# Performance work log

Measured on AMD Instinct MI355X. Metric: run time of the kernel, lower is better.

The kernel has to match this reference:

```python
import jax, jax.numpy as jnp
import numpy as np

ORDER = 2
BN_EPS = 1e-5

def setup_inputs() -> dict:
    key = jax.random.key(0)
    ks = jax.random.split(key, 8)
    B, N, L, H = 32, 512, 12, 64
    S = 2                      # support_len
    OUT = 64                   # out_dim
    M = ORDER * S * H          # einsum middle dim = 256
    x = jax.random.normal(ks[0], (B, N, L, H), dtype=jnp.float32)
    # row-scaled random diffusion matrices to keep multi-hop propagation stable
    support = jax.random.uniform(ks[1], (S, N, N), dtype=jnp.float32) / N
    scale = 1.0 / M
    weight = scale * jax.random.normal(ks[2], (L, M, OUT), dtype=jnp.float32)
    eps = jnp.zeros((1,), dtype=jnp.float32)
    gamma = jnp.ones((OUT,), dtype=jnp.float32)
    beta = jnp.zeros((OUT,), dtype=jnp.float32)
    w2 = jax.random.normal(ks[3], (OUT, OUT), dtype=jnp.float32) / np.sqrt(OUT)
    b2 = jnp.zeros((OUT,), dtype=jnp.float32)
    return {"x": x, "support": support, "weight": weight, "eps": eps,
            "gamma": gamma, "beta": beta, "w2": w2, "b2": b2}

def reference(x, support, weight, eps, gamma, beta, w2, b2):
    B, N, L, H = x.shape
    xv = x.reshape(B, N, L * H)            # [B,N,LH]
    res = []
    for i in range(support.shape[0]):      # small fixed loop over supports
        A = support[i]                     # [N,N]
        out = xv
        for _ in range(ORDER):
            out = (1.0 + eps) * out + jnp.einsum('nm,bmd->bnd', A, out)
            res.append(out)
    out = jnp.stack(res, axis=-1)          # [B,N,LH,K], K = order*support_len
    K = out.shape[-1]
    out = out.reshape(B, N, L, H * K)      # [B,N,L,M]
    out = jnp.einsum('bnlm,lmo->bno', out, weight)   # [B,N,OUT]
    # dropout is identity in eval mode
    C = out.shape[-1]
    flat = out.reshape(B * N, C)
    mean = flat.mean(axis=0)
    var = flat.var(axis=0)                 # biased, matching torch BN training
    normed = (flat - mean) * jax.lax.rsqrt(var + BN_EPS) * gamma + beta
    y = jax.nn.relu(normed.reshape(B, N, C))
    return jnp.einsum('bnc,oc->bno', y, w2) + b2
```

## Files before the change

kernel.cpp:

```cpp
#include <hip/hip_runtime.h>
#include <hip/hip_bf16.h>
#include <cstddef>
#include <cstdint>

#define B_   32
#define N_   512
#define D_   768
#define OUT_ 64
#define R_   (B_ * N_)

typedef unsigned short u16;
typedef __bf16 bf16x8 __attribute__((ext_vector_type(8)));
typedef float  f32x4  __attribute__((ext_vector_type(4)));
typedef unsigned short u16x8 __attribute__((ext_vector_type(8)));

__device__ __forceinline__ u16 f2bf(float f) {
    __hip_bfloat16 h = __float2bfloat16(f);
    return __builtin_bit_cast(u16, h);
}

__device__ __forceinline__ f32x4 mfma16(u16x8 a, u16x8 b, f32x4 c) {
    return __builtin_amdgcn_mfma_f32_16x16x32_bf16(
        __builtin_bit_cast(bf16x8, a), __builtin_bit_cast(bf16x8, b), c, 0, 0, 0);
}

__device__ __forceinline__ void gl2lds16(const void* g, void* l) {
    __builtin_amdgcn_global_load_lds(
        (const __attribute__((address_space(1))) unsigned int*)g,
        (__attribute__((address_space(3))) unsigned int*)l, 16, 0, 0);
}

__global__ __launch_bounds__(256) void prep2(
    const float* __restrict__ support, const float* __restrict__ weight,
    const float* __restrict__ epsp,
    u16* __restrict__ MallC, u16* __restrict__ MT, u16* __restrict__ Wt)
{
    const int blk = blockIdx.x, tid = threadIdx.x;
    __shared__ float t[32][33];
    if (blk < 512) {
        int s = blk >> 8, rem = blk & 255;
        int n0 = (rem >> 4) * 32, m0 = (rem & 15) * 32;
        const float f = 1.0f + epsp[0];
        const float* S = support + (size_t)s * 262144;
#pragma unroll
        for (int p = 0; p < 4; ++p) {
            int nl = p * 8 + (tid >> 5), ml = tid & 31;
            float v = S[(size_t)(n0 + nl) * 512 + m0 + ml];
            if (n0 + nl == m0 + ml) v += f;
            MallC[(size_t)(n0 + nl) * 2048 + s * 1024 + m0 + ml] = f2bf(v);
            t[nl][ml] = v;
        }
        __syncthreads();
#pragma unroll
        for (int p = 0; p < 4; ++p) {
            int ml = p * 8 + (tid >> 5), nl = tid & 31;
            MT[(size_t)s * 262144 + (size_t)(m0 + ml) * 512 + n0 + nl] = f2bf(t[nl][ml]);
        }
    } else {
        int idx = (blk - 512) * 256 + tid;
        int k = idx / 49152, rem = idx % 49152;
        int o = rem / 768, d = rem % 768;
        int l = d >> 6, hh = d & 63;
        Wt[idx] = f2bf(weight[((size_t)l * 256 + hh * 4 + k) * 64 + o]);
    }
}

__global__ __launch_bounds__(256, 4) void zmsq(
    const u16* __restrict__ Wt, const float* __restrict__ x,
    const u16* __restrict__ MallC_in, const u16* __restrict__ MT,
    u16* __restrict__ Z, u16* __restrict__ MallC_out)
{
    __shared__ __align__(16) u16 SM[16384];
    const int tid = threadIdx.x, lane = tid & 63, wid = tid >> 6;
    const int wr = wid >> 1, wc = wid & 1;
    const int lrow = lane & 15, lk8 = (lane >> 4) * 8;
    const int q = lane >> 4;
    const int bid = blockIdx.x;

    f32x4 acc[2][2] = {};

    if (bid < 1024) {
        const int k = (bid >> 3) & 3;
        const int r2 = (bid >> 5) * 8 + (bid & 7);
        const int b = r2 >> 3, m0 = (r2 & 7) * 64;

        const u16* gsrcA[2]; u16* ldstA[2];
#pragma unroll
        for (int t = 0; t < 2; ++t) {
            int idx = wid * 2 + t;
            int p = idx >> 2, sub = idx & 3;
            gsrcA[t] = Wt + (size_t)(k * 64 + sub * 16 + lrow) * 768 + p * 32 + lk8;
            ldstA[t] = SM + p * 2048 + sub * 512;
        }
        const int r = tid >> 2, c4 = tid & 3;
        const float* gx = x + (size_t)(b * 512 + m0 + r) * 768 + c4 * 16;
        u16* bdst = SM + 4096 + (c4 >> 1) * 2048 + (r >> 4) * 512
                  + (c4 & 1) * 256 + (r & 15) * 8;

        {
            f32x4 a0 = *(const f32x4*)(gx);
            f32x4 a1 = *(const f32x4*)(gx + 4);
            f32x4 a2 = *(const f32x4*)(gx + 8);
            f32x4 a3 = *(const f32x4*)(gx + 12);
#pragma unroll
            for (int t = 0; t < 2; ++t) gl2lds16(gsrcA[t], ldstA[t]);
            u16x8 w0, w1;
#pragma unroll
            for (int j = 0; j < 4; ++j) {
                w0[j] = f2bf(a0[j]); w0[4 + j] = f2bf(a1[j]);
                w1[j] = f2bf(a2[j]); w1[4 + j] = f2bf(a3[j]);
            }
            *(u16x8*)(bdst)       = w0;
            *(u16x8*)(bdst + 128) = w1;
        }
        __syncthreads();

#pragma unroll 2
        for (int kk = 0; kk < 12; ++kk) {
            const int cb = (kk & 1) * 8192, nb = cb ^ 8192;
            f32x4 a0, a1, a2, a3;
            if (kk < 11) {
                const float* g = gx + (kk + 1) * 64;
                a0 = *(const f32x4*)(g);
                a1 = *(const f32x4*)(g + 4);
                a2 = *(const f32x4*)(g + 8);
                a3 = *(const f32x4*)(g + 12);
#pragma unroll
                for (int t = 0; t < 2; ++t)
                    gl2lds16(gsrcA[t] + (kk + 1) * 64, ldstA[t] + nb);
            }
#pragma unroll
            for (int p = 0; p < 2; ++p) {
                u16x8 af[2], bq[2];
#pragma unroll
                for (int f = 0; f < 2; ++f)
                    af[f] = *(const u16x8*)(SM + cb + p * 2048 + (wr * 2 + f) * 512 + lane * 8);
#pragma unroll
                for (int f = 0; f < 2; ++f)
                    bq[f] = *(const u16x8*)(SM + cb + 4096 + p * 2048 + (wc * 2 + f) * 512 + lane * 8);
#pragma unroll
                for (int fi = 0; fi < 2; ++fi)
#pragma unroll
                    for (int fj = 0; fj < 2; ++fj)
                        acc[fi][fj] = mfma16(af[fi], bq[fj], acc[fi][fj]);
            }
            if (kk < 11) {
                u16x8 w0, w1;
#pragma unroll
                for (int j = 0; j < 4; ++j) {
                    w0[j] = f2bf(a0[j]); w0[4 + j] = f2bf(a1[j]);
                    w1[j] = f2bf(a2[j]); w1[4 + j] = f2bf(a3[j]);
                }
                *(u16x8*)(bdst + nb)       = w0;
                *(u16x8*)(bdst + nb + 128) = w1;
            }
            __syncthreads();
        }
        u16* Rw = SM + wid * 1280;
#pragma unroll
        for (int fi = 0; fi < 2; ++fi)
#pragma unroll
            for (int fj = 0; fj < 2; ++fj)
#pragma unroll
                for (int rr = 0; rr < 4; ++rr)
                    Rw[(fi * 16 + q * 4 + rr) * 40 + fj * 16 + lrow] = f2bf(acc[fi][fj][rr]);
        __syncthreads();
        const int r3 = lane >> 1, cc = (lane & 1) * 16;
        u16x8 v0 = *(const u16x8*)(Rw + r3 * 40 + cc);
        u16x8 v1 = *(const u16x8*)(Rw + r3 * 40 + cc + 8);
        u16* zp = Z + (size_t)(b * 64 + wr * 32 + r3) * 2048 + k * 512 + m0 + wc * 32 + cc;
        *(u16x8*)(zp)     = v0;
        *(u16x8*)(zp + 8) = v1;
    } else {
        const int lb = bid - 1024;
        const int s = lb >> 6, i0 = ((lb >> 3) & 7) * 64, j0 = (lb & 7) * 64;

        const u16* gsrc[4]; u16* ldst[4];
#pragma unroll
        for (int t = 0; t < 4; ++t) {
            int idx = wid * 4 + t;
            if (idx < 8) {
                int p = idx >> 2, sub = idx & 3;
                gsrc[t] = MallC_in + (size_t)(i0 + sub * 16 + lrow) * 2048 + s * 1024 + p * 32 + lk8;
                ldst[t] = SM + p * 2048 + sub * 512;
            } else {
                int i2 = idx - 8;
                int p = i2 >> 2, sub = i2 & 3;
                gsrc[t] = MT + (size_t)s * 262144 + (size_t)(j0 + sub * 16 + lrow) * 512 + p * 32 + lk8;
                ldst[t] = SM + 4096 + p * 2048 + sub * 512;
            }
        }
#pragma unroll
        for (int t = 0; t < 4; ++t) gl2lds16(gsrc[t], ldst[t]);
        __syncthreads();
#pragma unroll 2
        for (int kk = 0; kk < 8; ++kk) {
            const int cb = (kk & 1) * 8192, nb = cb ^ 8192;
            if (kk < 7) {
#pragma unroll
                for (int t = 0; t < 4; ++t)
                    gl2lds16(gsrc[t] + (kk + 1) * 64, ldst[t] + nb);
            }
#pragma unroll
            for (int p = 0; p < 2; ++p) {
                u16x8 af[2], bq[2];
#pragma unroll
                for (int f = 0; f < 2; ++f)
                    af[f] = *(const u16x8*)(SM + cb + p * 2048 + (wr * 2 + f) * 512 + lane * 8);
#pragma unroll
                for (int f = 0; f < 2; ++f)
                    bq[f] = *(const u16x8*)(SM + cb + 4096 + p * 2048 + (wc * 2 + f) * 512 + lane * 8);
#pragma unroll
                for (int fi = 0; fi < 2; ++fi)
#pragma unroll
                    for (int fj = 0; fj < 2; ++fj)
                        acc[fi][fj] = mfma16(af[fi], bq[fj], acc[fi][fj]);
            }
            __syncthreads();
        }
#pragma unroll
        for (int fi = 0; fi < 2; ++fi)
#pragma unroll
            for (int fj = 0; fj < 2; ++fj)
#pragma unroll
                for (int rr = 0; rr < 4; ++rr) {
                    int n = i0 + wr * 32 + fi * 16 + q * 4 + rr;
                    int c = j0 + wc * 32 + fj * 16 + lrow;
                    MallC_out[(size_t)n * 2048 + (2 * s + 1) * 512 + c] = f2bf(acc[fi][fj][rr]);
                }
    }
}

__global__ __launch_bounds__(256, 4) void ysum(
    const u16* __restrict__ G, const u16* __restrict__ Z, float* __restrict__ Yh)
{
    __shared__ __align__(16) u16 SM[16384];
    const int tid = threadIdx.x, lane = tid & 63, wid = tid >> 6;
    const int wr = wid >> 1, wc = wid & 1;
    const int lrow = lane & 15, lk8 = (lane >> 4) * 8;
    const int bid = blockIdx.x;
    const int kq = bid >> 8, rt = bid & 255;
    const int r0 = rt * 64, b = rt >> 3, n0 = r0 & 511;

    const u16* gsrc[4]; u16* ldst[4];
#pragma unroll
    for (int t = 0; t < 4; ++t) {
        int idx = wid * 4 + t;
        if (idx < 8) {
            int p = idx >> 2, sub = idx & 3;
            gsrc[t] = G + (size_t)(n0 + sub * 16 + lrow) * 2048 + kq * 512 + p * 32 + lk8;
            ldst[t] = SM + p * 2048 + sub * 512;
        } else {
            int i2 = idx - 8;
            int p = i2 >> 2, sub = i2 & 3;
            gsrc[t] = Z + (size_t)(b * 64 + sub * 16 + lrow) * 2048 + kq * 512 + p * 32 + lk8;
            ldst[t] = SM + 4096 + p * 2048 + sub * 512;
        }
    }
    f32x4 acc[2][2] = {};
#pragma unroll
    for (int t = 0; t < 4; ++t) gl2lds16(gsrc[t], ldst[t]);
    __syncthreads();
#pragma unroll 2
    for (int kk = 0; kk < 8; ++kk) {
        const int cb = (kk & 1) * 8192, nb = cb ^ 8192;
        if (kk < 7) {
#pragma unroll
            for (int t = 0; t < 4; ++t)
                gl2lds16(gsrc[t] + (kk + 1) * 64, ldst[t] + nb);
        }
#pragma unroll
        for (int p = 0; p < 2; ++p) {
            u16x8 af[2], bq[2];
#pragma unroll
            for (int f = 0; f < 2; ++f)
                af[f] = *(const u16x8*)(SM + cb + p * 2048 + (wr * 2 + f) * 512 + lane * 8);
#pragma unroll
            for (int f = 0; f < 2; ++f)
                bq[f] = *(const u16x8*)(SM + cb + 4096 + p * 2048 + (wc * 2 + f) * 512 + lane * 8);
#pragma unroll
            for (int fi = 0; fi < 2; ++fi)
#pragma unroll
                for (int fj = 0; fj < 2; ++fj)
                    acc[fi][fj] = mfma16(af[fi], bq[fj], acc[fi][fj]);
        }
        __syncthreads();
    }
    const int q = lane >> 4;
    float* Yk = Yh + (size_t)kq * R_ * 64;
#pragma unroll
    for (int fi = 0; fi < 2; ++fi)
#pragma unroll
        for (int fj = 0; fj < 2; ++fj)
#pragma unroll
            for (int rr = 0; rr < 4; ++rr) {
                int r2 = r0 + wr * 32 + fi * 16 + q * 4 + rr;
                int o  = wc * 32 + fj * 16 + lrow;
                Yk[(size_t)r2 * 64 + o] = acc[fi][fj][rr];
            }
}

__global__ __launch_bounds__(256) void bn_part(
    const float* __restrict__ Yh, float* __restrict__ part)
{
    const int blk = blockIdx.x, tid = threadIdx.x;
    const int o = tid & 63, g = tid >> 6;
    float s = 0.f, s2 = 0.f;
#pragma unroll
    for (int p = 0; p < 16; ++p) {
        int r = blk * 64 + p * 4 + g;
        size_t off = (size_t)r * 64 + o;
        float v = Yh[off] + Yh[(size_t)R_ * 64 + off]
                + Yh[(size_t)2 * R_ * 64 + off] + Yh[(size_t)3 * R_ * 64 + off];
        s += v; s2 += v * v;
    }
    __shared__ float ls[4][64], ls2[4][64];
    ls[g][o] = s; ls2[g][o] = s2;
    __syncthreads();
    if (tid < 64) {
        float t = 0.f, t2 = 0.f;
#pragma unroll
        for (int g2 = 0; g2 < 4; ++g2) { t += ls[g2][tid]; t2 += ls2[g2][tid]; }
        part[blk * 128 + tid]      = t;
        part[blk * 128 + 64 + tid] = t2;
    }
}

__global__ __launch_bounds__(256) void bn_out(
    const float* __restrict__ Yh, const float* __restrict__ part,
    const float* __restrict__ gamma, const float* __restrict__ beta,
    const float* __restrict__ w2, const float* __restrict__ b2,
    float* __restrict__ out)
{
    __shared__ float ys[64 * 68];
    __shared__ float w2s[64 * 65];
    __shared__ float red[4][64], red2[4][64];
    __shared__ float sa[64], sh[64];
    const int tid = threadIdx.x;
    const int r0 = blockIdx.x * 64;
    const int o = tid & 63, g = tid >> 6;
    {
        float s = 0.f, s2 = 0.f;
        for (int p = g; p < 256; p += 4) {
            s  += part[p * 128 + o];
            s2 += part[p * 128 + 64 + o];
        }
        red[g][o] = s; red2[g][o] = s2;
    }
#pragma unroll
    for (int i = 0; i < 16; ++i) {
        int idx = tid + i * 256;
        w2s[(idx >> 6) * 65 + (idx & 63)] = w2[idx];
    }
    __syncthreads();
    if (tid < 64) {
        float t0 = red[0][tid] + red[1][tid] + red[2][tid] + red[3][tid];
        float t2 = red2[0][tid] + red2[1][tid] + red2[2][tid] + red2[3][tid];
        float mean = t0 * (1.0f / R_);
        float var  = t2 * (1.0f / R_) - mean * mean;
        float a = rsqrtf(var + 1e-5f) * gamma[tid];
        sa[tid] = a;
        sh[tid] = beta[tid] - mean * a;
    }
    __syncthreads();
    {
        float a = sa[o], bsh = sh[o];
#pragma unroll
        for (int p = 0; p < 16; ++p) {
            int rl = p * 4 + g;
            size_t off = (size_t)(r0 + rl) * 64 + o;
            float v = Yh[off] + Yh[(size_t)R_ * 64 + off]
                    + Yh[(size_t)2 * R_ * 64 + off] + Yh[(size_t)3 * R_ * 64 + off];
            ys[o * 68 + rl] = fmaxf(fmaf(v, a, bsh), 0.f);
        }
    }
    __syncthreads();
    float acc[16];
    float bb = b2[o];
#pragma unroll
    for (int j = 0; j < 16; ++j) acc[j] = bb;
    for (int c = 0; c < 64; ++c) {
        float wv = w2s[o * 65 + c];
        const float* yr = ys + c * 68 + g * 16;
        f32x4 y0 = *(const f32x4*)(yr);
        f32x4 y1 = *(const f32x4*)(yr + 4);
        f32x4 y2 = *(const f32x4*)(yr + 8);
        f32x4 y3 = *(const f32x4*)(yr + 12);
#pragma unroll
        for (int j = 0; j < 4; ++j) {
            acc[j]      = fmaf(wv, y0[j], acc[j]);
            acc[4 + j]  = fmaf(wv, y1[j], acc[4 + j]);
            acc[8 + j]  = fmaf(wv, y2[j], acc[8 + j]);
            acc[12 + j] = fmaf(wv, y3[j], acc[12 + j]);
        }
    }
#pragma unroll
    for (int j = 0; j < 16; ++j)
        out[(size_t)(r0 + g * 16 + j) * OUT_ + o] = acc[j];
}

extern "C" void kernel_launch(void* const* d_in, const int* in_sizes, int n_in,
                              void* d_out, int out_size, void* d_ws, size_t ws_size,
                              hipStream_t stream)
{
    const float* x       = (const float*)d_in[0];
    const float* support = (const float*)d_in[1];
    const float* weight  = (const float*)d_in[2];
    const float* eps     = (const float*)d_in[3];
    const float* gamma   = (const float*)d_in[4];
    const float* beta    = (const float*)d_in[5];
    const float* w2      = (const float*)d_in[6];
    const float* b2      = (const float*)d_in[7];
    float* out = (float*)d_out;

    char* ws = (char*)d_ws;
    u16*   MallC = (u16*)(ws);
    u16*   MT    = (u16*)(ws + 2097152);
    u16*   Wt    = (u16*)(ws + 3145728);
    u16*   Z     = (u16*)(ws + 3538944);
    float* Yh    = (float*)(ws + 11927552);
    float* part  = (float*)(ws + 28704768);

    prep2  <<<1280, 256, 0, stream>>>(support, weight, eps, MallC, MT, Wt);
    zmsq   <<<1152, 256, 0, stream>>>(Wt, x, MallC, MT, Z, MallC);
    ysum   <<<1024, 256, 0, stream>>>(MallC, Z, Yh);
    bn_part<<<256,  256, 0, stream>>>(Yh, part);
    bn_out <<<256,  256, 0, stream>>>(Yh, part, gamma, beta, w2, b2, out);
}
```

Before: 168.3 us.

## Compute all four Z slices per block so each x tile is read once

The Z-computation branch of zmsq now has each block cover all 256 weight rows (4 k slices x 64 outputs) for a 64-row x tile, with a 4x4 MFMA tile per wave, instead of one block per k slice. The aim is to stop reading and converting the fp32 x tile to bf16 four times. In exchange, shared memory grows to 80KB per block, occupancy drops to 2 blocks per CU, and the grid shrinks from 1152 to 384 blocks. That risks under-filling the GPU and leaves less room to hide latency.

Measured after the change: 163.5 us. 2.9% less time.

```diff
diff --git a/kernel.cpp b/kernel.cpp
--- a/kernel.cpp
+++ b/kernel.cpp
@@ -65,37 +65,36 @@
     }
 }
 
-__global__ __launch_bounds__(256, 4) void zmsq(
+__global__ __launch_bounds__(256, 2) void zmsq(
     const u16* __restrict__ Wt, const float* __restrict__ x,
     const u16* __restrict__ MallC_in, const u16* __restrict__ MT,
     u16* __restrict__ Z, u16* __restrict__ MallC_out)
 {
-    __shared__ __align__(16) u16 SM[16384];
+    __shared__ __align__(16) u16 SM[40960];
     const int tid = threadIdx.x, lane = tid & 63, wid = tid >> 6;
-    const int wr = wid >> 1, wc = wid & 1;
     const int lrow = lane & 15, lk8 = (lane >> 4) * 8;
     const int q = lane >> 4;
     const int bid = blockIdx.x;
 
-    f32x4 acc[2][2] = {};
-
-    if (bid < 1024) {
-        const int k = (bid >> 3) & 3;
-        const int r2 = (bid >> 5) * 8 + (bid & 7);
-        const int b = r2 >> 3, m0 = (r2 & 7) * 64;
-
-        const u16* gsrcA[2]; u16* ldstA[2];
-#pragma unroll
-        for (int t = 0; t < 2; ++t) {
-            int idx = wid * 2 + t;
-            int p = idx >> 2, sub = idx & 3;
-            gsrcA[t] = Wt + (size_t)(k * 64 + sub * 16 + lrow) * 768 + p * 32 + lk8;
-            ldstA[t] = SM + p * 2048 + sub * 512;
+    if (bid < 256) {
+        const int b = bid >> 3, m0 = (bid & 7) * 64;
+        u16* Abuf = SM;
+        u16* Bbuf = SM + 32768;
+
+        const u16* gsrcA[8]; u16* ldstA[8];
+#pragma unroll
+        for (int t = 0; t < 8; ++t) {
+            int idx = wid * 8 + t;
+            int p = idx >> 4, g = idx & 15;
+            gsrcA[t] = Wt + (size_t)(g * 16 + lrow) * 768 + p * 32 + lk8;
+            ldstA[t] = Abuf + p * 8192 + g * 512;
         }
         const int r = tid >> 2, c4 = tid & 3;
         const float* gx = x + (size_t)(b * 512 + m0 + r) * 768 + c4 * 16;
-        u16* bdst = SM + 4096 + (c4 >> 1) * 2048 + (r >> 4) * 512
+        u16* bdst = Bbuf + (c4 >> 1) * 2048 + (r >> 4) * 512
                   + (c4 & 1) * 256 + (r & 15) * 8;
+
+        f32x4 acc[4][4] = {};
 
         {
             f32x4 a0 = *(const f32x4*)(gx);
@@ -103,7 +102,7 @@
             f32x4 a2 = *(const f32x4*)(gx + 8);
             f32x4 a3 = *(const f32x4*)(gx + 12);
 #pragma unroll
-            for (int t = 0; t < 2; ++t) gl2lds16(gsrcA[t], ldstA[t]);
+            for (int t = 0; t < 8; ++t) gl2lds16(gsrcA[t], ldstA[t]);
             u16x8 w0, w1;
 #pragma unroll
             for (int j = 0; j < 4; ++j) {
@@ -117,7 +116,8 @@
 
 #pragma unroll 2
         for (int kk = 0; kk < 12; ++kk) {
-            const int cb = (kk & 1) * 8192, nb = cb ^ 8192;
+            const int cbA = (kk & 1) * 16384, nbA = cbA ^ 16384;
+            const int cbB = (kk & 1) * 4096,  nbB = cbB ^ 4096;
             f32x4 a0, a1, a2, a3;
             if (kk < 11) {
                 const float* g = gx + (kk + 1) * 64;
@@ -126,22 +126,22 @@
                 a2 = *(const f32x4*)(g + 8);
                 a3 = *(const f32x4*)(g + 12);
 #pragma unroll
-                for (int t = 0; t < 2; ++t)
-                    gl2lds16(gsrcA[t] + (kk + 1) * 64, ldstA[t] + nb);
+                for (int t = 0; t < 8; ++t)
+                    gl2lds16(gsrcA[t] + (kk + 1) * 64, ldstA[t] + nbA);
             }
 #pragma unroll
             for (int p = 0; p < 2; ++p) {
-                u16x8 af[2], bq[2];
-#pragma unroll
-                for (int f = 0; f < 2; ++f)
-                    af[f] = *(const u16x8*)(SM + cb + p * 2048 + (wr * 2 + f) * 512 + lane * 8);
-#pragma unroll
-                for (int f = 0; f < 2; ++f)
-                    bq[f] = *(const u16x8*)(SM + cb + 4096 + p * 2048 + (wc * 2 + f) * 512 + lane * 8);
-#pragma unroll
-                for (int fi = 0; fi < 2; ++fi)
-#pragma unroll
-                    for (int fj = 0; fj < 2; ++fj)
+                u16x8 af[4], bq[4];
+#pragma unroll
+                for (int f = 0; f < 4; ++f)
+                    af[f] = *(const u16x8*)(Abuf + cbA + p * 8192 + (wid * 4 + f) * 512 + lane * 8);
+#pragma unroll
+                for (int f = 0; f < 4; ++f)
+                    bq[f] = *(const u16x8*)(Bbuf + cbB + p * 2048 + f * 512 + lane * 8);
+#pragma unroll
+                for (int fi = 0; fi < 4; ++fi)
+#pragma unroll
+                    for (int fj = 0; fj < 4; ++fj)
                         acc[fi][fj] = mfma16(af[fi], bq[fj], acc[fi][fj]);
             }
             if (kk < 11) {
@@ -151,29 +151,34 @@
                     w0[j] = f2bf(a0[j]); w0[4 + j] = f2bf(a1[j]);
                     w1[j] = f2bf(a2[j]); w1[4 + j] = f2bf(a3[j]);
                 }
-                *(u16x8*)(bdst + nb)       = w0;
-                *(u16x8*)(bdst + nb + 128) = w1;
+                *(u16x8*)(bdst + nbB)       = w0;
+                *(u16x8*)(bdst + nbB + 128) = w1;
             }
             __syncthreads();
         }
-        u16* Rw = SM + wid * 1280;
-#pragma unroll
-        for (int fi = 0; fi < 2; ++fi)
-#pragma unroll
-            for (int fj = 0; fj < 2; ++fj)
+
+        u16* scr = SM;
+#pragma unroll
+        for (int fi = 0; fi < 4; ++fi)
+#pragma unroll
+            for (int fj = 0; fj < 4; ++fj)
 #pragma unroll
                 for (int rr = 0; rr < 4; ++rr)
-                    Rw[(fi * 16 + q * 4 + rr) * 40 + fj * 16 + lrow] = f2bf(acc[fi][fj][rr]);
+                    scr[(wid * 64 + fi * 16 + q * 4 + rr) * 72 + fj * 16 + lrow]
+                        = f2bf(acc[fi][fj][rr]);
         __syncthreads();
-        const int r3 = lane >> 1, cc = (lane & 1) * 16;
-        u16x8 v0 = *(const u16x8*)(Rw + r3 * 40 + cc);
-        u16x8 v1 = *(const u16x8*)(Rw + r3 * 40 + cc + 8);
-        u16* zp = Z + (size_t)(b * 64 + wr * 32 + r3) * 2048 + k * 512 + m0 + wc * 32 + cc;
-        *(u16x8*)(zp)     = v0;
-        *(u16x8*)(zp + 8) = v1;
+        const int c8 = (tid & 7) * 8, rg = tid >> 3;
+#pragma unroll
+        for (int i = 0; i < 8; ++i) {
+            int srow = i * 32 + rg;
+            u16x8 v = *(const u16x8*)(scr + srow * 72 + c8);
+            int o = srow & 63, k = srow >> 6;
+            *(u16x8*)(Z + (size_t)(b * 64 + o) * 2048 + k * 512 + m0 + c8) = v;
+        }
     } else {
-        const int lb = bid - 1024;
+        const int lb = bid - 256;
         const int s = lb >> 6, i0 = ((lb >> 3) & 7) * 64, j0 = (lb & 7) * 64;
+        const int wr = wid >> 1, wc = wid & 1;
 
         const u16* gsrc[4]; u16* ldst[4];
 #pragma unroll
@@ -190,6 +195,7 @@
                 ldst[t] = SM + 4096 + p * 2048 + sub * 512;
             }
         }
+        f32x4 acc[2][2] = {};
 #pragma unroll
         for (int t = 0; t < 4; ++t) gl2lds16(gsrc[t], ldst[t]);
         __syncthreads();
@@ -422,7 +428,7 @@
     float* part  = (float*)(ws + 28704768);
 
     prep2  <<<1280, 256, 0, stream>>>(support, weight, eps, MallC, MT, Wt);
-    zmsq   <<<1152, 256, 0, stream>>>(Wt, x, MallC, MT, Z, MallC);
+    zmsq   <<<384,  256, 0, stream>>>(Wt, x, MallC, MT, Z, MallC);
     ysum   <<<1024, 256, 0, stream>>>(MallC, Z, Yh);
     bn_part<<<256,  256, 0, stream>>>(Yh, part);
     bn_out <<<256,  256, 0, stream>>>(Yh, part, gamma, beta, w2, b2, out);
```
